# Kernel tuning notes

Measured on AMD Instinct MI355X. Metric: run time of the kernel, lower is better.

Reference implementation:

```python
import jax, jax.numpy as jnp
import numpy as np

B, T, E, HD = 8, 2048, 1024, 64  # batch, seq (== n_ctx), n_embd, head_dim = n_embd // n_head


def setup_inputs() -> dict:
    key = jax.random.key(0)
    k1, k2, k3, k4 = jax.random.split(key, 4)
    x = jax.random.normal(k1, (B, T, E), dtype=jnp.float32)
    s = E ** -0.5  # Linear-like init scale
    Wq = jax.random.normal(k2, (E, HD), dtype=jnp.float32) * s
    Wk = jax.random.normal(k3, (E, HD), dtype=jnp.float32) * s
    Wv = jax.random.normal(k4, (E, HD), dtype=jnp.float32) * s
    return {"x": x, "Wq": Wq, "Wk": Wk, "Wv": Wv}


def reference(x, Wq, Wk, Wv):
    # q,k,v: [B, T, HD]
    q = jnp.einsum('bte,eh->bth', x, Wq)
    k = jnp.einsum('bte,eh->bth', x, Wk)
    v = jnp.einsum('bte,eh->bth', x, Wv)
    scale = k.shape[-1] ** -0.5
    # scores: [B, T, T]
    alpha = jnp.einsum('bqh,bkh->bqk', q, k) * scale
    causal = jnp.tril(jnp.ones((T, T), dtype=bool))
    alpha = jnp.where(causal, alpha, -jnp.inf)
    alpha = jax.nn.softmax(alpha, axis=-1)
    # dropout with p=0.0 is identity in eval
    h = jnp.einsum('bqk,bkh->bqh', alpha, v)  # [B, T, HD]
    return h
```

## Files before the change

kernel.cpp:

```cpp
#include <hip/hip_runtime.h>
#include <hip/hip_bf16.h>
#include <math.h>

#define BATCH 8
#define T 2048
#define E 1024
#define HD 64
#define BT (BATCH * T)

typedef __bf16 bf16_t;
typedef bf16_t bf16x4 __attribute__((ext_vector_type(4)));
typedef bf16_t bf16x8 __attribute__((ext_vector_type(8)));
typedef float f32x4 __attribute__((ext_vector_type(4)));

#define MFMA(a, b, c) __builtin_amdgcn_mfma_f32_16x16x32_bf16((a), (b), (c), 0, 0, 0)

#define QSCALE (0.125f * 1.44269504088896340736f)


__global__ __launch_bounds__(256) void prep_w(const float* __restrict__ Wq,
                                              const float* __restrict__ Wk,
                                              const float* __restrict__ Wv,
                                              bf16_t* __restrict__ WTt) {
    const int nt  = blockIdx.x >> 3;
    const int kc0 = (blockIdx.x & 7) * 128;
    const int tid = threadIdx.x;
    const int l16 = tid & 15;
    const int k8  = (kc0 >> 3) + (tid >> 4);
    const int n   = nt * 16 + l16;
    const int m   = n >> 6;
    const int col = n & 63;
    const float* W = (m == 0) ? Wq : (m == 1) ? Wk : Wv;
    const float scale = (m == 0) ? QSCALE : 1.0f;
    bf16x8 o;
#pragma unroll
    for (int j = 0; j < 8; j++) {
        o[j] = (bf16_t)(W[(size_t)(k8 * 8 + j) * HD + col] * scale);
    }
    *reinterpret_cast<bf16x8*>(WTt + (size_t)nt * 16384 + k8 * 128 + l16 * 8) = o;
}

__global__ __launch_bounds__(256, 4) void qkv_proj(
    const float* __restrict__ x,
    const bf16_t* __restrict__ WTt,
    bf16_t* __restrict__ qt,
    bf16_t* __restrict__ kt,
    bf16_t* __restrict__ vt)
{
    __shared__ __align__(16) bf16_t xbuf[2][32][72];

    const int tid  = threadIdx.x;
    const int wave = tid >> 6;
    const int lane = tid & 63;
    const int l16  = lane & 15;
    const int quad = lane >> 4;
    const int wr   = wave >> 1;
    const int wc   = wave & 1;
    const int rowbase0 = blockIdx.x * 32;

    const int srow = tid >> 3;
    const int sseg = tid & 7;
    const float* xsrc = x + (size_t)(rowbase0 + srow) * E + sseg * 8;

    f32x4 acc[6] = {};

    {
        f32x4 xa = *reinterpret_cast<const f32x4*>(xsrc);
        f32x4 xb = *reinterpret_cast<const f32x4*>(xsrc + 4);
        bf16x8 xw;
#pragma unroll
        for (int u = 0; u < 4; u++) {
            xw[u]     = (bf16_t)xa[u];
            xw[4 + u] = (bf16_t)xb[u];
        }
        *reinterpret_cast<bf16x8*>(&xbuf[0][srow][sseg * 8]) = xw;
    }
    __syncthreads();

    int p = 0;
    for (int kc = 0; kc < E; kc += 64) {
        const int kn = (kc + 64) & (E - 1);
        const f32x4 nxa = *reinterpret_cast<const f32x4*>(xsrc + kn);
        const f32x4 nxb = *reinterpret_cast<const f32x4*>(xsrc + kn + 4);

        bf16x8 bf[2][6];
#pragma unroll
        for (int ks = 0; ks < 2; ks++) {
#pragma unroll
            for (int tc = 0; tc < 6; tc++) {
                bf[ks][tc] = *reinterpret_cast<const bf16x8*>(
                    WTt + (size_t)(wc * 6 + tc) * 16384 + (kc + ks * 32) * 16 + lane * 8);
            }
        }

        const bf16x8 a0 = *reinterpret_cast<const bf16x8*>(&xbuf[p][wr * 16 + l16][quad * 8]);
        const bf16x8 a1 = *reinterpret_cast<const bf16x8*>(&xbuf[p][wr * 16 + l16][32 + quad * 8]);

#pragma unroll
        for (int tc = 0; tc < 6; tc++) acc[tc] = MFMA(a0, bf[0][tc], acc[tc]);
#pragma unroll
        for (int tc = 0; tc < 6; tc++) acc[tc] = MFMA(a1, bf[1][tc], acc[tc]);

        bf16x8 xw;
#pragma unroll
        for (int u = 0; u < 4; u++) {
            xw[u]     = (bf16_t)nxa[u];
            xw[4 + u] = (bf16_t)nxb[u];
        }
        *reinterpret_cast<bf16x8*>(&xbuf[p ^ 1][srow][sseg * 8]) = xw;
        __syncthreads();
        p ^= 1;
    }

    const int rowbase = rowbase0 + wr * 16;
#pragma unroll
    for (int tc = 0; tc < 6; tc++) {
        const int n0  = wc * 96 + tc * 16;
        const int m   = n0 >> 6;
        const int tcg = (n0 & 63) >> 4;
        if (m < 2) {
            bf16_t* dst = (m == 0) ? qt : kt;
            const size_t o0 = (size_t)(rowbase >> 4) * 1024 +
                              (size_t)(tcg * 2 + (l16 >> 3)) * 128 + (l16 & 7);
#pragma unroll
            for (int r = 0; r < 4; r++) {
                dst[o0 + (quad * 4 + r) * 8] = (bf16_t)acc[tc][r];
            }
        } else {
            const int b_    = rowbase >> 11;
            const int tbase = rowbase & (T - 1);
            const size_t o0 = (size_t)b_ * 131072 +
                              (size_t)((tbase >> 3) + (quad >> 1)) * 128 +
                              l16 * 8 + (quad & 1) * 4 + (size_t)tcg * 32768;
            bf16x4 pv;
#pragma unroll
            for (int r = 0; r < 4; r++) pv[r] = (bf16_t)acc[tc][r];
            *reinterpret_cast<bf16x4*>(vt + o0) = pv;
        }
    }
}

__global__ __launch_bounds__(512) void attn(
    const bf16_t* __restrict__ qtl,
    const bf16_t* __restrict__ ktl,
    const bf16_t* __restrict__ vtl,
    float* __restrict__ out)
{
    __shared__ __align__(16) bf16_t plds[8][16][40];
    __shared__ float opart[8][16][66];
    __shared__ float lpart[8][16];

    const int wave = threadIdx.x >> 6;
    const int lane = threadIdx.x & 63;
    const int l16  = lane & 15;
    const int quad = lane >> 4;
    const int group = wave >> 2;
    const int kw    = wave & 3;

    const int b  = blockIdx.x >> 6;
    const int pr = blockIdx.x & 63;
    const int qt = group ? (127 - pr) : pr;
    const int rowbase = qt * 16;

    const bf16_t* Qb = qtl + (size_t)((b * T + rowbase) >> 4) * 1024 + lane * 8;
    const bf16_t* Kb = ktl + (size_t)b * T * 64 + lane * 8;
    const bf16_t* Vb = vtl + (size_t)b * 131072 + lane * 8;

    const bf16x8 qf0 = *reinterpret_cast<const bf16x8*>(Qb);
    const bf16x8 qf1 = *reinterpret_cast<const bf16x8*>(Qb + 512);

    f32x4 o[4] = {};
    f32x4 lrun = {};

    const int nch = (rowbase + 47) >> 5;

    int k0 = kw * 32;
    bf16x8 kfa0 = *reinterpret_cast<const bf16x8*>(Kb + k0 * 64);
    bf16x8 kfb0 = *reinterpret_cast<const bf16x8*>(Kb + k0 * 64 + 512);
    bf16x8 kfa1 = *reinterpret_cast<const bf16x8*>(Kb + k0 * 64 + 1024);
    bf16x8 kfb1 = *reinterpret_cast<const bf16x8*>(Kb + k0 * 64 + 1536);
    bf16x8 vf0 = *reinterpret_cast<const bf16x8*>(Vb + k0 * 16);
    bf16x8 vf1 = *reinterpret_cast<const bf16x8*>(Vb + k0 * 16 + 32768);
    bf16x8 vf2 = *reinterpret_cast<const bf16x8*>(Vb + k0 * 16 + 65536);
    bf16x8 vf3 = *reinterpret_cast<const bf16x8*>(Vb + k0 * 16 + 98304);

    for (int c = kw; c < nch; c += 4) {
        k0 = c * 32;
        const int cn = (c + 4 < nch) ? (c + 4) : c;
        const int kn = cn * 32;
        bf16x8 nkfa0 = *reinterpret_cast<const bf16x8*>(Kb + kn * 64);
        bf16x8 nkfb0 = *reinterpret_cast<const bf16x8*>(Kb + kn * 64 + 512);
        bf16x8 nkfa1 = *reinterpret_cast<const bf16x8*>(Kb + kn * 64 + 1024);
        bf16x8 nkfb1 = *reinterpret_cast<const bf16x8*>(Kb + kn * 64 + 1536);
        bf16x8 nvf0 = *reinterpret_cast<const bf16x8*>(Vb + kn * 16);
        bf16x8 nvf1 = *reinterpret_cast<const bf16x8*>(Vb + kn * 16 + 32768);
        bf16x8 nvf2 = *reinterpret_cast<const bf16x8*>(Vb + kn * 16 + 65536);
        bf16x8 nvf3 = *reinterpret_cast<const bf16x8*>(Vb + kn * 16 + 98304);

        f32x4 s_lo = {};
        f32x4 s_hi = {};
        s_lo = MFMA(qf0, kfa0, s_lo);
        s_lo = MFMA(qf1, kfb0, s_lo);
        s_hi = MFMA(qf0, kfa1, s_hi);
        s_hi = MFMA(qf1, kfb1, s_hi);

        if (k0 + 31 > rowbase) {
            const int row = rowbase + quad * 4;
#pragma unroll
            for (int r = 0; r < 4; r++) {
                if (k0 + l16 > row + r)      s_lo[r] = -INFINITY;
                if (k0 + 16 + l16 > row + r) s_hi[r] = -INFINITY;
            }
        }

#pragma unroll
        for (int r = 0; r < 4; r++) {
            const float p0 = exp2f(s_lo[r]);
            const float p1 = exp2f(s_hi[r]);
            lrun[r] += p0 + p1;
            plds[wave][quad * 4 + r][l16]      = (bf16_t)p0;
            plds[wave][quad * 4 + r][16 + l16] = (bf16_t)p1;
        }
        const bf16x8 pf = *reinterpret_cast<const bf16x8*>(&plds[wave][l16][quad * 8]);

        o[0] = MFMA(pf, vf0, o[0]);
        o[1] = MFMA(pf, vf1, o[1]);
        o[2] = MFMA(pf, vf2, o[2]);
        o[3] = MFMA(pf, vf3, o[3]);

        kfa0 = nkfa0; kfb0 = nkfb0; kfa1 = nkfa1; kfb1 = nkfb1;
        vf0 = nvf0; vf1 = nvf1; vf2 = nvf2; vf3 = nvf3;
    }

#pragma unroll
    for (int r = 0; r < 4; r++) {
        float l = lrun[r];
        l += __shfl_xor(l, 1);
        l += __shfl_xor(l, 2);
        l += __shfl_xor(l, 4);
        l += __shfl_xor(l, 8);
        if (l16 == 0) lpart[wave][quad * 4 + r] = l;
#pragma unroll
        for (int nb = 0; nb < 4; nb++) {
            opart[wave][quad * 4 + r][nb * 16 + l16] = o[nb][r];
        }
    }
    __syncthreads();

    const int g    = threadIdx.x >> 8;
    const int gtid = threadIdx.x & 255;
    const int qtg  = g ? (127 - pr) : pr;
    const size_t outbase = (size_t)b * T + qtg * 16;
#pragma unroll
    for (int pass = 0; pass < 4; pass++) {
        const int row = pass * 4 + (gtid >> 6);
        const int col = gtid & 63;
        float osum = 0.f, lsum = 0.f;
#pragma unroll
        for (int w = 0; w < 4; w++) {
            osum += opart[g * 4 + w][row][col];
            lsum += lpart[g * 4 + w][row];
        }
        out[(outbase + row) * HD + col] = osum / lsum;
    }
}

extern "C" void kernel_launch(void* const* d_in, const int* in_sizes, int n_in,
                              void* d_out, int out_size, void* d_ws, size_t ws_size,
                              hipStream_t stream) {
    const float* x  = (const float*)d_in[0];
    const float* Wq = (const float*)d_in[1];
    const float* Wk = (const float*)d_in[2];
    const float* Wv = (const float*)d_in[3];
    float* out = (float*)d_out;

    bf16_t* ws  = (bf16_t*)d_ws;
    bf16_t* WTt = ws;
    bf16_t* qtl = WTt + (size_t)192 * E;
    bf16_t* ktl = qtl + (size_t)BT * HD;
    bf16_t* vtl = ktl + (size_t)BT * HD;

    prep_w<<<96, 256, 0, stream>>>(Wq, Wk, Wv, WTt);
    qkv_proj<<<512, 256, 0, stream>>>(x, WTt, qtl, ktl, vtl);
    attn<<<512, 512, 0, stream>>>(qtl, ktl, vtl, out);
}
```

Baseline: 131.0 us.

## Load x straight into MFMA registers and prefetch weight fragments a step ahead

The QKV projection drops its LDS double buffer and block-wide barriers. Each lane now reads its own x fragment from global memory and converts it to bf16 in registers. Weight fragments are software-prefetched one k-step ahead, alongside the x prefetch. This removes shared-memory traffic and __syncthreads stalls, but each x row is now loaded by both column waves, and the extra live registers led to relaxing the launch-bounds occupancy hint.

```diff
diff --git a/kernel.cpp b/kernel.cpp
--- a/kernel.cpp
+++ b/kernel.cpp
@@ -40,15 +40,13 @@
     *reinterpret_cast<bf16x8*>(WTt + (size_t)nt * 16384 + k8 * 128 + l16 * 8) = o;
 }
 
-__global__ __launch_bounds__(256, 4) void qkv_proj(
+__global__ __launch_bounds__(256) void qkv_proj(
     const float* __restrict__ x,
     const bf16_t* __restrict__ WTt,
     bf16_t* __restrict__ qt,
     bf16_t* __restrict__ kt,
     bf16_t* __restrict__ vt)
 {
-    __shared__ __align__(16) bf16_t xbuf[2][32][72];
-
     const int tid  = threadIdx.x;
     const int wave = tid >> 6;
     const int lane = tid & 63;
@@ -58,58 +56,61 @@
     const int wc   = wave & 1;
     const int rowbase0 = blockIdx.x * 32;
 
-    const int srow = tid >> 3;
-    const int sseg = tid & 7;
-    const float* xsrc = x + (size_t)(rowbase0 + srow) * E + sseg * 8;
+    const float* xr = x + (size_t)(rowbase0 + wr * 16 + l16) * E + quad * 8;
+    const bf16_t* Bb = WTt + (size_t)(wc * 6) * 16384 + lane * 8;
 
     f32x4 acc[6] = {};
 
-    {
-        f32x4 xa = *reinterpret_cast<const f32x4*>(xsrc);
-        f32x4 xb = *reinterpret_cast<const f32x4*>(xsrc + 4);
-        bf16x8 xw;
-#pragma unroll
-        for (int u = 0; u < 4; u++) {
-            xw[u]     = (bf16_t)xa[u];
-            xw[4 + u] = (bf16_t)xb[u];
-        }
-        *reinterpret_cast<bf16x8*>(&xbuf[0][srow][sseg * 8]) = xw;
-    }
-    __syncthreads();
-
-    int p = 0;
+    f32x4 xa0 = *reinterpret_cast<const f32x4*>(xr);
+    f32x4 xb0 = *reinterpret_cast<const f32x4*>(xr + 4);
+    f32x4 xa1 = *reinterpret_cast<const f32x4*>(xr + 32);
+    f32x4 xb1 = *reinterpret_cast<const f32x4*>(xr + 36);
+    bf16x8 bcur[2][6];
+#pragma unroll
+    for (int ks = 0; ks < 2; ks++) {
+#pragma unroll
+        for (int tc = 0; tc < 6; tc++) {
+            bcur[ks][tc] = *reinterpret_cast<const bf16x8*>(
+                Bb + (size_t)tc * 16384 + (ks * 32) * 16);
+        }
+    }
+
     for (int kc = 0; kc < E; kc += 64) {
         const int kn = (kc + 64) & (E - 1);
-        const f32x4 nxa = *reinterpret_cast<const f32x4*>(xsrc + kn);
-        const f32x4 nxb = *reinterpret_cast<const f32x4*>(xsrc + kn + 4);
-
-        bf16x8 bf[2][6];
+        const f32x4 nxa0 = *reinterpret_cast<const f32x4*>(xr + kn);
+        const f32x4 nxb0 = *reinterpret_cast<const f32x4*>(xr + kn + 4);
+        const f32x4 nxa1 = *reinterpret_cast<const f32x4*>(xr + kn + 32);
+        const f32x4 nxb1 = *reinterpret_cast<const f32x4*>(xr + kn + 36);
+        bf16x8 bn[2][6];
 #pragma unroll
         for (int ks = 0; ks < 2; ks++) {
 #pragma unroll
             for (int tc = 0; tc < 6; tc++) {
-                bf[ks][tc] = *reinterpret_cast<const bf16x8*>(
-                    WTt + (size_t)(wc * 6 + tc) * 16384 + (kc + ks * 32) * 16 + lane * 8);
+                bn[ks][tc] = *reinterpret_cast<const bf16x8*>(
+                    Bb + (size_t)tc * 16384 + (kn + ks * 32) * 16);
             }
         }
 
-        const bf16x8 a0 = *reinterpret_cast<const bf16x8*>(&xbuf[p][wr * 16 + l16][quad * 8]);
-        const bf16x8 a1 = *reinterpret_cast<const bf16x8*>(&xbuf[p][wr * 16 + l16][32 + quad * 8]);
-
-#pragma unroll
-        for (int tc = 0; tc < 6; tc++) acc[tc] = MFMA(a0, bf[0][tc], acc[tc]);
-#pragma unroll
-        for (int tc = 0; tc < 6; tc++) acc[tc] = MFMA(a1, bf[1][tc], acc[tc]);
-
-        bf16x8 xw;
+        bf16x8 a0, a1;
 #pragma unroll
         for (int u = 0; u < 4; u++) {
-            xw[u]     = (bf16_t)nxa[u];
-            xw[4 + u] = (bf16_t)nxb[u];
-        }
-        *reinterpret_cast<bf16x8*>(&xbuf[p ^ 1][srow][sseg * 8]) = xw;
-        __syncthreads();
-        p ^= 1;
+            a0[u]     = (bf16_t)xa0[u];
+            a0[4 + u] = (bf16_t)xb0[u];
+            a1[u]     = (bf16_t)xa1[u];
+            a1[4 + u] = (bf16_t)xb1[u];
+        }
+
+#pragma unroll
+        for (int tc = 0; tc < 6; tc++) acc[tc] = MFMA(a0, bcur[0][tc], acc[tc]);
+#pragma unroll
+        for (int tc = 0; tc < 6; tc++) acc[tc] = MFMA(a1, bcur[1][tc], acc[tc]);
+
+        xa0 = nxa0; xb0 = nxb0; xa1 = nxa1; xb1 = nxb1;
+#pragma unroll
+        for (int ks = 0; ks < 2; ks++) {
+#pragma unroll
+            for (int tc = 0; tc < 6; tc++) bcur[ks][tc] = bn[ks][tc];
+        }
     }
 
     const int rowbase = rowbase0 + wr * 16;
```

New measurement: 144.2 us. 1.1x slower.
